# Optimization experiments

Hardware: AMD Instinct MI355X
Metric: run time of the kernel (lower is better)

Reference implementation:

```python
import jax, jax.numpy as jnp
import numpy as np

B, L, D, H = 8, 1500, 1024, 8
HD = D // H
N_BOUNDARIES = 300  # exactly 300 boundaries per sequence -> max_segments = 300
EPS = 1e-5


def setup_inputs() -> dict:
    key = jax.random.key(0)
    ks = jax.random.split(key, 6)
    rng = np.random.default_rng(0)
    boundaries = np.zeros((B, L), dtype=np.float32)
    for b in range(B):
        boundaries[b, rng.permutation(L)[:N_BOUNDARIES]] = 1.0
    lengths = rng.uniform(0.5, 1.0, size=(B,)).astype(np.float32)
    hidden = jax.random.normal(ks[0], (B, L, D), jnp.float32)
    learned_query = jax.random.normal(ks[1], (D,), jnp.float32) * 0.02
    eye = jnp.eye(D, dtype=jnp.float32)
    # identity-initialized projections, perturbed so the test is non-trivial
    Wk = eye + 0.02 * jax.random.normal(ks[2], (D, D), jnp.float32)
    Wv = eye + 0.02 * jax.random.normal(ks[3], (D, D), jnp.float32)
    Wo = eye + 0.02 * jax.random.normal(ks[4], (D, D), jnp.float32)
    return {
        'hidden': hidden,
        'boundaries': jnp.asarray(boundaries),
        'lengths': jnp.asarray(lengths),
        'learned_query': learned_query,
        'Wk': Wk, 'Wv': Wv, 'Wo': Wo,
        'ln_gamma': jnp.ones((D,), jnp.float32),
        'ln_beta': jnp.zeros((D,), jnp.float32),
        'max_segments': N_BOUNDARIES,
    }


def _attention_pooling(hidden, boundaries, lengths, learned_query, Wk, Wv, Wo,
                       ln_gamma, ln_beta, max_segments):
    # segment id per token: cumsum(b) - b (token before first boundary -> seg 0)
    seg_id = jnp.cumsum(boundaries, axis=1) - boundaries            # (B, L)
    # foo[b,t,s] = s - seg_id[b,t]; foo == 0 -> token t belongs to segment s
    seg_mask = (jnp.arange(max_segments)[None, None, :] == seg_id[:, :, None])
    actual_lens = (lengths * L).astype(jnp.int32)                   # (B,)
    len_mask = jnp.arange(L)[None, :] < actual_lens[:, None]        # (B, L)
    seg_mask = seg_mask & len_mask[:, :, None]                      # (B, L, S) bool

    # LayerNorm (biased variance, as torch.nn.LayerNorm)
    mu = jnp.mean(hidden, axis=-1, keepdims=True)
    var = jnp.var(hidden, axis=-1, keepdims=True)
    hn = (hidden - mu) * jax.lax.rsqrt(var + EPS) * ln_gamma + ln_beta

    k = (hn @ Wk.T).reshape(B, L, H, HD)
    v = (hn @ Wv.T).reshape(B, L, H, HD)
    q = learned_query.reshape(H, HD)
    # queries are the same learned vector for every segment -> compute (B,H,L)
    # once and broadcast across S (same math as the original dense matmul)
    scores = jnp.einsum('hd,blhd->bhl', q, k) * (HD ** -0.5)        # (B, H, L)

    mask = seg_mask.transpose(0, 2, 1)[:, None, :, :]               # (B, 1, S, L)
    scores4 = jnp.where(mask, scores[:, :, None, :], -1e30)         # (B, H, S, L)
    w = jax.nn.softmax(scores4, axis=-1)
    w = jnp.where(mask, w, 0.0)
    # rows with no valid token: softmax of all -inf -> nan_to_num(0) in torch
    row_valid = jnp.any(mask, axis=-1, keepdims=True)
    w = jnp.where(row_valid, w, 0.0)

    pooled = jnp.einsum('bhsl,blhd->bshd', w, v).reshape(B, max_segments, D)
    return pooled @ Wo.T                                            # (B, S, D)


def reference(hidden, boundaries, lengths, learned_query, Wk, Wv, Wo,
              ln_gamma, ln_beta, max_segments):
    return _attention_pooling(hidden, boundaries, lengths, learned_query,
                              Wk, Wv, Wo, ln_gamma, ln_beta, max_segments)
```

## Files before the change

kernel.cpp:

```cpp
#include <hip/hip_runtime.h>
#include <hip/hip_bf16.h>

#define BPK_B 8
#define BPK_L 1500
#define BPK_D 1024
#define BPK_H 8
#define BPK_S 300
#define BPK_EPS 1e-5f
#define BPK_M (BPK_B * BPK_L)
#define BPK_MS (BPK_B * BPK_S)
#define BPK_HP_ROWS 2432
#define BPK_PO_PAD 2560

typedef __hip_bfloat16 bf16;
typedef __bf16 bf16x8 __attribute__((ext_vector_type(8)));
typedef float v4f __attribute__((ext_vector_type(4)));

static __device__ __forceinline__ float bf_lo(unsigned u) {
    return __uint_as_float((u & 0xffffu) << 16);
}
static __device__ __forceinline__ float bf_hi(unsigned u) {
    return __uint_as_float((u >> 16) << 16);
}
static __device__ __forceinline__ void bpk_store(float v, float* p) { *p = v; }
static __device__ __forceinline__ void bpk_store(float v, bf16* p) { *p = __float2bfloat16(v); }
static __device__ __forceinline__ uint2 pack4bf(float a, float b, float c, float d) {
    union { bf16 h[4]; uint2 u; } pk;
    pk.h[0] = __float2bfloat16(a); pk.h[1] = __float2bfloat16(b);
    pk.h[2] = __float2bfloat16(c); pk.h[3] = __float2bfloat16(d);
    return pk.u;
}

#define BPK_GL2LDS(gsrc, ldst)                                                 \
    __builtin_amdgcn_global_load_lds(                                          \
        (const __attribute__((address_space(1))) void*)(gsrc),                 \
        (__attribute__((address_space(3))) void*)(ldst), 16, 0, 0)

__global__ __launch_bounds__(256) void bpk_prep_kernel(
    const float* __restrict__ lq, const float* __restrict__ Wk,
    const float* __restrict__ boundaries, const float* __restrict__ lengths,
    bf16* __restrict__ qkb, int* __restrict__ seg_start, int* __restrict__ seg_cnt) {
    __shared__ unsigned char flags[1536];
    __shared__ int st_sh[BPK_S + 2];
    __shared__ int wsumi[4];
    int blk = blockIdx.x;
    int tid = threadIdx.x;
    if (blk < 32) {
        int o = blk * 256 + tid;
        int h = o >> 10, k = o & 1023;
        const float* wr = Wk + (size_t)(h * 128) * BPK_D + k;
        const float* qr = lq + h * 128;
        float s = 0.f;
        #pragma unroll 8
        for (int d = 0; d < 128; d++)
            s += qr[d] * wr[(size_t)d * BPK_D];
        qkb[o] = __float2bfloat16(s);
        return;
    }
    int b = blk - 32;
    int alen = (int)(lengths[b] * (float)BPK_L);
    const float* bd = boundaries + (size_t)b * BPK_L;
    for (int t = tid; t < 1536; t += 256)
        flags[t] = (t < BPK_L && bd[t] >= 0.5f) ? 1 : 0;
    for (int s = tid; s < BPK_S + 2; s += 256) st_sh[s] = BPK_L;
    __syncthreads();
    int base = tid * 6;
    int lsum = 0;
    #pragma unroll
    for (int j = 0; j < 6; j++) lsum += flags[base + j];
    int lane = tid & 63, wid = tid >> 6;
    int scan = lsum;
    #pragma unroll
    for (int off = 1; off < 64; off <<= 1) {
        int u = __shfl_up(scan, off);
        if (lane >= off) scan += u;
    }
    if (lane == 63) wsumi[wid] = scan;
    __syncthreads();
    int wbase = 0;
    for (int w = 0; w < wid; w++) wbase += wsumi[w];
    int run = wbase + scan - lsum;
    #pragma unroll
    for (int j = 0; j < 6; j++) {
        int t = base + j;
        if (t < BPK_L) {
            int sid = run;
            if ((t == 0 || flags[t - 1]) && sid <= BPK_S) st_sh[sid] = t;
            if (flags[t]) run++;
        }
    }
    __syncthreads();
    for (int s = tid; s < BPK_S; s += 256) {
        int st = st_sh[s];
        int e = min(st_sh[s + 1], alen);
        int s0 = min(st, alen);
        seg_start[b * BPK_S + s] = st;
        seg_cnt[b * BPK_S + s] = max(0, e - s0);
    }
}

__global__ __launch_bounds__(256) void bpk_ln_score_conv_kernel(
    const float* __restrict__ x, const float* __restrict__ gamma,
    const float* __restrict__ beta, const bf16* __restrict__ qkb,
    const float* __restrict__ lengths,
    const float* __restrict__ Wv, const float* __restrict__ Wo,
    bf16* __restrict__ wvb, bf16* __restrict__ wob,
    float2* __restrict__ murs, float* __restrict__ scores) {
    int tid = threadIdx.x;
    if (blockIdx.x >= 1024) {
        int cb = blockIdx.x - 1024;
        const float* s = cb < 1024 ? Wv : Wo;
        bf16* d = cb < 1024 ? wvb : wob;
        int i = ((cb & 1023) * 256 + tid) * 4;
        float4 v = *(const float4*)(s + i);
        *(uint2*)(d + i) = pack4bf(v.x, v.y, v.z, v.w);
        return;
    }
    int lane = tid & 63, wid = tid >> 6;
    float4 g[4], bb[4];
    uint2 qk[8][4];
    #pragma unroll
    for (int j = 0; j < 4; j++) {
        g[j]  = *(const float4*)(gamma + j * 256 + lane * 4);
        bb[j] = *(const float4*)(beta + j * 256 + lane * 4);
    }
    #pragma unroll
    for (int h = 0; h < 8; h++)
        #pragma unroll
        for (int j = 0; j < 4; j++)
            qk[h][j] = *(const uint2*)(qkb + h * BPK_D + j * 256 + lane * 4);
    float lv = (lane < BPK_B) ? lengths[lane] : 0.f;
    const bool b0 = (lane & 1) != 0;
    const bool b1 = (lane & 2) != 0;
    const bool b2 = (lane & 4) != 0;
    const int head = 4 * (lane & 1) + (lane & 2) + ((lane >> 2) & 1);

    const int nwaves = 1024 * 4;
    for (int row = blockIdx.x * 4 + wid; row < BPK_M; row += nwaves) {
        int b = row / BPK_L, t = row - b * BPK_L;
        float alenf = __shfl(lv, b);
        if (t >= (int)(alenf * (float)BPK_L)) continue;
        const float* xr = x + (size_t)row * BPK_D;
        float4 f[4];
        float s = 0.f, sq = 0.f;
        #pragma unroll
        for (int j = 0; j < 4; j++) {
            f[j] = *(const float4*)(xr + j * 256 + lane * 4);
            s  += f[j].x + f[j].y + f[j].z + f[j].w;
            sq += f[j].x * f[j].x + f[j].y * f[j].y
                + f[j].z * f[j].z + f[j].w * f[j].w;
        }
        #pragma unroll
        for (int off = 1; off < 64; off <<= 1) {
            s  += __shfl_xor(s, off);
            sq += __shfl_xor(sq, off);
        }
        float mu = s * (1.0f / BPK_D);
        float var = sq * (1.0f / BPK_D) - mu * mu;
        float rs = rsqrtf(var + BPK_EPS);
        float p[8];
        #pragma unroll
        for (int h = 0; h < 8; h++) p[h] = 0.f;
        #pragma unroll
        for (int j = 0; j < 4; j++) {
            float h0 = (f[j].x - mu) * rs * g[j].x + bb[j].x;
            float h1 = (f[j].y - mu) * rs * g[j].y + bb[j].y;
            float h2 = (f[j].z - mu) * rs * g[j].z + bb[j].z;
            float h3 = (f[j].w - mu) * rs * g[j].w + bb[j].w;
            #pragma unroll
            for (int h = 0; h < 8; h++) {
                uint2 qv = qk[h][j];
                p[h] += h0 * bf_lo(qv.x) + h1 * bf_hi(qv.x)
                      + h2 * bf_lo(qv.y) + h3 * bf_hi(qv.y);
            }
        }
        #pragma unroll
        for (int r = 0; r < 4; r++) {
            float send = b0 ? p[r] : p[r + 4];
            float recv = __shfl_xor(send, 1);
            p[r]     += b0 ? 0.f : recv;
            p[r + 4] += b0 ? recv : 0.f;
        }
        float q0 = b0 ? p[4] : p[0];
        float q1 = b0 ? p[5] : p[1];
        float q2 = b0 ? p[6] : p[2];
        float q3 = b0 ? p[7] : p[3];
        {
            float send = b1 ? q0 : q2;
            float recv = __shfl_xor(send, 2);
            q0 += b1 ? 0.f : recv;
            q2 += b1 ? recv : 0.f;
            send = b1 ? q1 : q3;
            recv = __shfl_xor(send, 2);
            q1 += b1 ? 0.f : recv;
            q3 += b1 ? recv : 0.f;
        }
        float a = b1 ? q2 : q0;
        float c = b1 ? q3 : q1;
        float send = b2 ? a : c;
        float recv = __shfl_xor(send, 4);
        float v = (b2 ? c : a) + recv;
        v += __shfl_xor(v, 8);
        v += __shfl_xor(v, 16);
        v += __shfl_xor(v, 32);
        if (lane < 8) {
            scores[((size_t)b * BPK_H + head) * BPK_L + t] =
                v * 0.088388347648318447f;
        } else if (lane == 8) {
            murs[row] = make_float2(mu, rs);
        }
    }
}

__global__ __launch_bounds__(256) void bpk_pool_kernel(
    const float* __restrict__ scores, const float* __restrict__ x,
    const float* __restrict__ gamma, const float* __restrict__ beta,
    const float2* __restrict__ murs,
    const int* __restrict__ seg_start, const int* __restrict__ seg_cnt,
    bf16* __restrict__ hpool) {
    int bs = blockIdx.x;
    int b = bs / BPK_S;
    int tid = threadIdx.x;
    int lane = tid & 63, wid = tid >> 6;
    __shared__ float minv[8][2];
    __shared__ float wls[8][128];
    int cnt = seg_cnt[bs], st = seg_start[bs];
    float4 g4 = *(const float4*)(gamma + tid * 4);
    float4 b4 = *(const float4*)(beta + tid * 4);
    float acc[8][4];
    #pragma unroll
    for (int h = 0; h < 8; h++)
        #pragma unroll
        for (int j = 0; j < 4; j++) acc[h][j] = 0.f;
    if (cnt > 0) {
        if (wid == 0) {
            int h = lane & 7, i0 = lane >> 3;
            const float* sc = scores + ((size_t)(b * 8 + h)) * BPK_L + st;
            float m = -1e30f;
            for (int i = i0; i < cnt; i += 8) m = fmaxf(m, sc[i]);
            #pragma unroll
            for (int off = 8; off < 64; off <<= 1) m = fmaxf(m, __shfl_xor(m, off));
            float l = 0.f;
            for (int i = i0; i < cnt; i += 8) l += __expf(sc[i] - m);
            #pragma unroll
            for (int off = 8; off < 64; off <<= 1) l += __shfl_xor(l, off);
            if (i0 == 0) { minv[h][0] = m; minv[h][1] = 1.0f / l; }
        }
        __syncthreads();
        for (int cb = 0; cb < cnt; cb += 128) {
            int cc = min(128, cnt - cb);
            int hh = tid >> 5, i0 = (tid & 31) * 4;
            #pragma unroll
            for (int j = 0; j < 4; j++) {
                int i = i0 + j;
                if (i < cc)
                    wls[hh][i] = __expf(scores[((size_t)(b * 8 + hh)) * BPK_L + st + cb + i]
                                        - minv[hh][0]) * minv[hh][1];
            }
            __syncthreads();
            const float* xp = x + (size_t)(b * BPK_L + st + cb) * BPK_D + tid * 4;
            const float2* mp = murs + (size_t)(b * BPK_L + st + cb);
            for (int i = 0; i < cc; i++) {
                float4 f = *(const float4*)(xp + (size_t)i * BPK_D);
                float2 mr = mp[i];
                float x0 = (f.x - mr.x) * mr.y * g4.x + b4.x;
                float x1 = (f.y - mr.x) * mr.y * g4.y + b4.y;
                float x2 = (f.z - mr.x) * mr.y * g4.z + b4.z;
                float x3 = (f.w - mr.x) * mr.y * g4.w + b4.w;
                #pragma unroll
                for (int h = 0; h < 8; h++) {
                    float w = wls[h][i];
                    acc[h][0] += w * x0; acc[h][1] += w * x1;
                    acc[h][2] += w * x2; acc[h][3] += w * x3;
                }
            }
            __syncthreads();
        }
    }
    #pragma unroll
    for (int h = 0; h < 8; h++)
        *(uint2*)(hpool + ((size_t)h * BPK_HP_ROWS + bs) * BPK_D + tid * 4) =
            pack4bf(acc[h][0], acc[h][1], acc[h][2], acc[h][3]);
}

__global__ __launch_bounds__(256) void bpk_headgemm_kernel(
    const bf16* __restrict__ hpool, const bf16* __restrict__ wvb,
    bf16* __restrict__ pooled) {
    const int mt = blockIdx.x >> 1, nt = blockIdx.x & 1, h = blockIdx.y;
    const int m0 = mt * 64, n0 = nt * 64;
    const bf16* A = hpool + (size_t)h * BPK_HP_ROWS * BPK_D;
    const bf16* W = wvb + (size_t)(h * 128 + n0) * BPK_D;
    __shared__ bf16 As[64][32];
    __shared__ bf16 Bs[64][32];
    const int tid = threadIdx.x;
    const int lane = tid & 63, wid = tid >> 6;
    const int wm = (wid & 1) * 32, wn = (wid >> 1) * 32;
    const int lm = lane & 15, quad = lane >> 4;
    const int rA = wid * 16 + (lane >> 2);
    const int colc = (lane & 3) * 8;

    v4f acc[2][2];
    #pragma unroll
    for (int i = 0; i < 2; i++)
        #pragma unroll
        for (int j = 0; j < 2; j++) acc[i][j] = (v4f){0.f, 0.f, 0.f, 0.f};

    for (int k0 = 0; k0 < BPK_D; k0 += 32) {
        BPK_GL2LDS(&A[(size_t)(m0 + rA) * BPK_D + k0 + colc], &As[wid * 16][0]);
        BPK_GL2LDS(&W[(size_t)rA * BPK_D + k0 + colc], &Bs[wid * 16][0]);
        __syncthreads();
        bf16x8 af[2], bfr[2];
        #pragma unroll
        for (int i = 0; i < 2; i++)
            af[i] = *(const bf16x8*)&As[wm + i * 16 + lm][quad * 8];
        #pragma unroll
        for (int j = 0; j < 2; j++)
            bfr[j] = *(const bf16x8*)&Bs[wn + j * 16 + lm][quad * 8];
        #pragma unroll
        for (int i = 0; i < 2; i++)
            #pragma unroll
            for (int j = 0; j < 2; j++)
                acc[i][j] = __builtin_amdgcn_mfma_f32_16x16x32_bf16(af[i], bfr[j], acc[i][j], 0, 0, 0);
        __syncthreads();
    }
    #pragma unroll
    for (int i = 0; i < 2; i++) {
        int mbase = m0 + wm + i * 16 + quad * 4;
        #pragma unroll
        for (int j = 0; j < 2; j++) {
            int col = h * 128 + n0 + wn + j * 16 + lm;
            #pragma unroll
            for (int r = 0; r < 4; r++) {
                int m = mbase + r;
                if (m < BPK_MS)
                    pooled[(size_t)m * BPK_D + col] = __float2bfloat16(acc[i][j][r]);
            }
        }
    }
}

__global__ __launch_bounds__(256) void bpk_ogemm_kernel(
    const bf16* __restrict__ A, const bf16* __restrict__ W,
    float* __restrict__ O) {
    const int flat = blockIdx.x;
    const int xcd = flat & 7, slot = flat >> 3;
    const int mt = xcd + 8 * (slot >> 4);
    const int nt = slot & 15;
    const int m0 = mt * 64, n0 = nt * 64;
    __shared__ bf16 As[64][32];
    __shared__ bf16 Bs[64][32];
    const int tid = threadIdx.x;
    const int lane = tid & 63, wid = tid >> 6;
    const int wm = (wid & 1) * 32, wn = (wid >> 1) * 32;
    const int lm = lane & 15, quad = lane >> 4;
    const int rA = wid * 16 + (lane >> 2);
    const int colc = (lane & 3) * 8;

    v4f acc[2][2];
    #pragma unroll
    for (int i = 0; i < 2; i++)
        #pragma unroll
        for (int j = 0; j < 2; j++) acc[i][j] = (v4f){0.f, 0.f, 0.f, 0.f};

    for (int k0 = 0; k0 < BPK_D; k0 += 32) {
        BPK_GL2LDS(&A[(size_t)(m0 + rA) * BPK_D + k0 + colc], &As[wid * 16][0]);
        BPK_GL2LDS(&W[(size_t)(n0 + rA) * BPK_D + k0 + colc], &Bs[wid * 16][0]);
        __syncthreads();
        bf16x8 af[2], bfr[2];
        #pragma unroll
        for (int i = 0; i < 2; i++)
            af[i] = *(const bf16x8*)&As[wm + i * 16 + lm][quad * 8];
        #pragma unroll
        for (int j = 0; j < 2; j++)
            bfr[j] = *(const bf16x8*)&Bs[wn + j * 16 + lm][quad * 8];
        #pragma unroll
        for (int i = 0; i < 2; i++)
            #pragma unroll
            for (int j = 0; j < 2; j++)
                acc[i][j] = __builtin_amdgcn_mfma_f32_16x16x32_bf16(af[i], bfr[j], acc[i][j], 0, 0, 0);
        __syncthreads();
    }
    #pragma unroll
    for (int i = 0; i < 2; i++) {
        int mbase = m0 + wm + i * 16 + quad * 4;
        #pragma unroll
        for (int j = 0; j < 2; j++) {
            int col = n0 + wn + j * 16 + lm;
            #pragma unroll
            for (int r = 0; r < 4; r++) {
                int m = mbase + r;
                if (m < BPK_MS) O[(size_t)m * BPK_D + col] = acc[i][j][r];
            }
        }
    }
}

extern "C" void kernel_launch(void* const* d_in, const int* in_sizes, int n_in,
                              void* d_out, int out_size, void* d_ws, size_t ws_size,
                              hipStream_t stream) {
    const float* hidden     = (const float*)d_in[0];
    const float* boundaries = (const float*)d_in[1];
    const float* lengths    = (const float*)d_in[2];
    const float* lq         = (const float*)d_in[3];
    const float* Wk         = (const float*)d_in[4];
    const float* Wv         = (const float*)d_in[5];
    const float* Wo         = (const float*)d_in[6];
    const float* gamma      = (const float*)d_in[7];
    const float* beta       = (const float*)d_in[8];
    float* out              = (float*)d_out;

    char* ws = (char*)d_ws;
    size_t off = 0;
    auto carve = [&](size_t bytes) -> char* {
        char* p = ws + off;
        off += (bytes + 255) & ~(size_t)255;
        return p;
    };
    bf16* hpool    = (bf16*)carve((size_t)BPK_H * BPK_HP_ROWS * BPK_D * sizeof(bf16));
    bf16* pooled   = (bf16*)carve((size_t)BPK_PO_PAD * BPK_D * sizeof(bf16));
    bf16* wvb      = (bf16*)carve((size_t)BPK_D * BPK_D * sizeof(bf16));
    bf16* wob      = (bf16*)carve((size_t)BPK_D * BPK_D * sizeof(bf16));
    bf16* qkb      = (bf16*)carve((size_t)BPK_H * BPK_D * sizeof(bf16));
    float* scores  = (float*)carve((size_t)BPK_B * BPK_H * BPK_L * sizeof(float));
    float2* murs   = (float2*)carve((size_t)BPK_M * sizeof(float2));
    int* seg_start = (int*)carve((size_t)BPK_B * BPK_S * sizeof(int));
    int* seg_cnt   = (int*)carve((size_t)BPK_B * BPK_S * sizeof(int));

    bpk_prep_kernel<<<dim3(40), dim3(256), 0, stream>>>(
        lq, Wk, boundaries, lengths, qkb, seg_start, seg_cnt);
    bpk_ln_score_conv_kernel<<<dim3(3072), dim3(256), 0, stream>>>(
        hidden, gamma, beta, qkb, lengths, Wv, Wo, wvb, wob, murs, scores);
    bpk_pool_kernel<<<dim3(BPK_MS), dim3(256), 0, stream>>>(
        scores, hidden, gamma, beta, murs, seg_start, seg_cnt, hpool);
    bpk_headgemm_kernel<<<dim3(76, BPK_H), dim3(256), 0, stream>>>(
        hpool, wvb, pooled);
    bpk_ogemm_kernel<<<dim3(640), dim3(256), 0, stream>>>(
        pooled, wob, out);
}
```

Baseline: 173.9 us.

## Fuse LayerNorm/score kernel into per-segment pooling with online softmax

Merges the LayerNorm+score kernel and the segment pooling kernel into one kernel. Each segment block now computes LN statistics and per-head scores for its own tokens, keeps them in shared memory, and applies a chunked online softmax. This removes one launch and the global round trip for scores and mean/rstd. In exchange each block copies qk into LDS and reads hidden rows twice, and the weight-conversion blocks now share the same launch.

Result: slower. 218.1 us (+25.4%).

```diff
diff --git a/kernel.cpp b/kernel.cpp
--- a/kernel.cpp
+++ b/kernel.cpp
@@ -22,8 +22,6 @@
 static __device__ __forceinline__ float bf_hi(unsigned u) {
     return __uint_as_float((u >> 16) << 16);
 }
-static __device__ __forceinline__ void bpk_store(float v, float* p) { *p = v; }
-static __device__ __forceinline__ void bpk_store(float v, bf16* p) { *p = __float2bfloat16(v); }
 static __device__ __forceinline__ uint2 pack4bf(float a, float b, float c, float d) {
     union { bf16 h[4]; uint2 u; } pk;
     pk.h[0] = __float2bfloat16(a); pk.h[1] = __float2bfloat16(b);
@@ -99,16 +97,16 @@
     }
 }
 
-__global__ __launch_bounds__(256) void bpk_ln_score_conv_kernel(
+__global__ __launch_bounds__(256) void bpk_lnpool_kernel(
     const float* __restrict__ x, const float* __restrict__ gamma,
     const float* __restrict__ beta, const bf16* __restrict__ qkb,
-    const float* __restrict__ lengths,
     const float* __restrict__ Wv, const float* __restrict__ Wo,
     bf16* __restrict__ wvb, bf16* __restrict__ wob,
-    float2* __restrict__ murs, float* __restrict__ scores) {
+    const int* __restrict__ seg_start, const int* __restrict__ seg_cnt,
+    bf16* __restrict__ hpool) {
     int tid = threadIdx.x;
-    if (blockIdx.x >= 1024) {
-        int cb = blockIdx.x - 1024;
+    if (blockIdx.x >= BPK_MS) {
+        int cb = blockIdx.x - BPK_MS;
         const float* s = cb < 1024 ? Wv : Wo;
         bf16* d = cb < 1024 ? wvb : wob;
         int i = ((cb & 1023) * 256 + tid) * 4;
@@ -116,171 +114,170 @@
         *(uint2*)(d + i) = pack4bf(v.x, v.y, v.z, v.w);
         return;
     }
-    int lane = tid & 63, wid = tid >> 6;
-    float4 g[4], bb[4];
-    uint2 qk[8][4];
-    #pragma unroll
-    for (int j = 0; j < 4; j++) {
-        g[j]  = *(const float4*)(gamma + j * 256 + lane * 4);
-        bb[j] = *(const float4*)(beta + j * 256 + lane * 4);
-    }
-    #pragma unroll
-    for (int h = 0; h < 8; h++)
-        #pragma unroll
-        for (int j = 0; j < 4; j++)
-            qk[h][j] = *(const uint2*)(qkb + h * BPK_D + j * 256 + lane * 4);
-    float lv = (lane < BPK_B) ? lengths[lane] : 0.f;
-    const bool b0 = (lane & 1) != 0;
-    const bool b1 = (lane & 2) != 0;
-    const bool b2 = (lane & 4) != 0;
-    const int head = 4 * (lane & 1) + (lane & 2) + ((lane >> 2) & 1);
-
-    const int nwaves = 1024 * 4;
-    for (int row = blockIdx.x * 4 + wid; row < BPK_M; row += nwaves) {
-        int b = row / BPK_L, t = row - b * BPK_L;
-        float alenf = __shfl(lv, b);
-        if (t >= (int)(alenf * (float)BPK_L)) continue;
-        const float* xr = x + (size_t)row * BPK_D;
-        float4 f[4];
-        float s = 0.f, sq = 0.f;
-        #pragma unroll
-        for (int j = 0; j < 4; j++) {
-            f[j] = *(const float4*)(xr + j * 256 + lane * 4);
-            s  += f[j].x + f[j].y + f[j].z + f[j].w;
-            sq += f[j].x * f[j].x + f[j].y * f[j].y
-                + f[j].z * f[j].z + f[j].w * f[j].w;
-        }
-        #pragma unroll
-        for (int off = 1; off < 64; off <<= 1) {
-            s  += __shfl_xor(s, off);
-            sq += __shfl_xor(sq, off);
-        }
-        float mu = s * (1.0f / BPK_D);
-        float var = sq * (1.0f / BPK_D) - mu * mu;
-        float rs = rsqrtf(var + BPK_EPS);
-        float p[8];
-        #pragma unroll
-        for (int h = 0; h < 8; h++) p[h] = 0.f;
-        #pragma unroll
-        for (int j = 0; j < 4; j++) {
-            float h0 = (f[j].x - mu) * rs * g[j].x + bb[j].x;
-            float h1 = (f[j].y - mu) * rs * g[j].y + bb[j].y;
-            float h2 = (f[j].z - mu) * rs * g[j].z + bb[j].z;
-            float h3 = (f[j].w - mu) * rs * g[j].w + bb[j].w;
-            #pragma unroll
-            for (int h = 0; h < 8; h++) {
-                uint2 qv = qk[h][j];
-                p[h] += h0 * bf_lo(qv.x) + h1 * bf_hi(qv.x)
-                      + h2 * bf_lo(qv.y) + h3 * bf_hi(qv.y);
-            }
-        }
-        #pragma unroll
-        for (int r = 0; r < 4; r++) {
-            float send = b0 ? p[r] : p[r + 4];
-            float recv = __shfl_xor(send, 1);
-            p[r]     += b0 ? 0.f : recv;
-            p[r + 4] += b0 ? recv : 0.f;
-        }
-        float q0 = b0 ? p[4] : p[0];
-        float q1 = b0 ? p[5] : p[1];
-        float q2 = b0 ? p[6] : p[2];
-        float q3 = b0 ? p[7] : p[3];
-        {
-            float send = b1 ? q0 : q2;
-            float recv = __shfl_xor(send, 2);
-            q0 += b1 ? 0.f : recv;
-            q2 += b1 ? recv : 0.f;
-            send = b1 ? q1 : q3;
-            recv = __shfl_xor(send, 2);
-            q1 += b1 ? 0.f : recv;
-            q3 += b1 ? recv : 0.f;
-        }
-        float a = b1 ? q2 : q0;
-        float c = b1 ? q3 : q1;
-        float send = b2 ? a : c;
-        float recv = __shfl_xor(send, 4);
-        float v = (b2 ? c : a) + recv;
-        v += __shfl_xor(v, 8);
-        v += __shfl_xor(v, 16);
-        v += __shfl_xor(v, 32);
-        if (lane < 8) {
-            scores[((size_t)b * BPK_H + head) * BPK_L + t] =
-                v * 0.088388347648318447f;
-        } else if (lane == 8) {
-            murs[row] = make_float2(mu, rs);
-        }
-    }
-}
-
-__global__ __launch_bounds__(256) void bpk_pool_kernel(
-    const float* __restrict__ scores, const float* __restrict__ x,
-    const float* __restrict__ gamma, const float* __restrict__ beta,
-    const float2* __restrict__ murs,
-    const int* __restrict__ seg_start, const int* __restrict__ seg_cnt,
-    bf16* __restrict__ hpool) {
+    __shared__ bf16 qks[BPK_H * BPK_D];
+    __shared__ float sch[8][128];
+    __shared__ float mch[128][2];
+    __shared__ float wls[8][128];
+    __shared__ float mstate[8], lstate[8], asc[8], csum[8];
     int bs = blockIdx.x;
     int b = bs / BPK_S;
-    int tid = threadIdx.x;
     int lane = tid & 63, wid = tid >> 6;
-    __shared__ float minv[8][2];
-    __shared__ float wls[8][128];
-    int cnt = seg_cnt[bs], st = seg_start[bs];
+    for (int i = tid; i < (BPK_H * BPK_D) / 8; i += 256)
+        ((uint4*)qks)[i] = ((const uint4*)qkb)[i];
+    float4 gw[4], bw[4];
+    #pragma unroll
+    for (int j = 0; j < 4; j++) {
+        gw[j] = *(const float4*)(gamma + j * 256 + lane * 4);
+        bw[j] = *(const float4*)(beta + j * 256 + lane * 4);
+    }
     float4 g4 = *(const float4*)(gamma + tid * 4);
     float4 b4 = *(const float4*)(beta + tid * 4);
+    int cnt = seg_cnt[bs], st = seg_start[bs];
     float acc[8][4];
     #pragma unroll
     for (int h = 0; h < 8; h++)
         #pragma unroll
         for (int j = 0; j < 4; j++) acc[h][j] = 0.f;
-    if (cnt > 0) {
+    if (tid < 8) { mstate[tid] = -3.0e38f; lstate[tid] = 0.f; }
+    const bool bb0 = (lane & 1) != 0;
+    const bool bb1 = (lane & 2) != 0;
+    const bool bb2 = (lane & 4) != 0;
+    const int head = 4 * (lane & 1) + (lane & 2) + ((lane >> 2) & 1);
+    __syncthreads();
+
+    for (int c0 = 0; c0 < cnt; c0 += 128) {
+        int cc = min(128, cnt - c0);
+        for (int i = wid; i < cc; i += 4) {
+            const float* xr = x + (size_t)(b * BPK_L + st + c0 + i) * BPK_D;
+            float4 f[4];
+            float s = 0.f, sq = 0.f;
+            #pragma unroll
+            for (int j = 0; j < 4; j++) {
+                f[j] = *(const float4*)(xr + j * 256 + lane * 4);
+                s  += f[j].x + f[j].y + f[j].z + f[j].w;
+                sq += f[j].x * f[j].x + f[j].y * f[j].y
+                    + f[j].z * f[j].z + f[j].w * f[j].w;
+            }
+            #pragma unroll
+            for (int off = 1; off < 64; off <<= 1) {
+                s  += __shfl_xor(s, off);
+                sq += __shfl_xor(sq, off);
+            }
+            float mu = s * (1.0f / BPK_D);
+            float var = sq * (1.0f / BPK_D) - mu * mu;
+            float rs = rsqrtf(var + BPK_EPS);
+            float p[8];
+            #pragma unroll
+            for (int h = 0; h < 8; h++) p[h] = 0.f;
+            #pragma unroll
+            for (int j = 0; j < 4; j++) {
+                float h0 = (f[j].x - mu) * rs * gw[j].x + bw[j].x;
+                float h1 = (f[j].y - mu) * rs * gw[j].y + bw[j].y;
+                float h2 = (f[j].z - mu) * rs * gw[j].z + bw[j].z;
+                float h3 = (f[j].w - mu) * rs * gw[j].w + bw[j].w;
+                #pragma unroll
+                for (int h = 0; h < 8; h++) {
+                    uint2 qv = *(const uint2*)(qks + h * BPK_D + j * 256 + lane * 4);
+                    p[h] += h0 * bf_lo(qv.x) + h1 * bf_hi(qv.x)
+                          + h2 * bf_lo(qv.y) + h3 * bf_hi(qv.y);
+                }
+            }
+            #pragma unroll
+            for (int r = 0; r < 4; r++) {
+                float send = bb0 ? p[r] : p[r + 4];
+                float recv = __shfl_xor(send, 1);
+                p[r]     += bb0 ? 0.f : recv;
+                p[r + 4] += bb0 ? recv : 0.f;
+            }
+            float q0 = bb0 ? p[4] : p[0];
+            float q1 = bb0 ? p[5] : p[1];
+            float q2 = bb0 ? p[6] : p[2];
+            float q3 = bb0 ? p[7] : p[3];
+            {
+                float send = bb1 ? q0 : q2;
+                float recv = __shfl_xor(send, 2);
+                q0 += bb1 ? 0.f : recv;
+                q2 += bb1 ? recv : 0.f;
+                send = bb1 ? q1 : q3;
+                recv = __shfl_xor(send, 2);
+                q1 += bb1 ? 0.f : recv;
+                q3 += bb1 ? recv : 0.f;
+            }
+            float a = bb1 ? q2 : q0;
+            float c = bb1 ? q3 : q1;
+            float send = bb2 ? a : c;
+            float recv = __shfl_xor(send, 4);
+            float v = (bb2 ? c : a) + recv;
+            v += __shfl_xor(v, 8);
+            v += __shfl_xor(v, 16);
+            v += __shfl_xor(v, 32);
+            if (lane < 8) sch[head][i] = v * 0.088388347648318447f;
+            else if (lane == 8) { mch[i][0] = mu; mch[i][1] = rs; }
+        }
+        __syncthreads();
         if (wid == 0) {
             int h = lane & 7, i0 = lane >> 3;
-            const float* sc = scores + ((size_t)(b * 8 + h)) * BPK_L + st;
-            float m = -1e30f;
-            for (int i = i0; i < cnt; i += 8) m = fmaxf(m, sc[i]);
+            float m = -3.0e38f;
+            for (int i = i0; i < cc; i += 8) m = fmaxf(m, sch[h][i]);
             #pragma unroll
             for (int off = 8; off < 64; off <<= 1) m = fmaxf(m, __shfl_xor(m, off));
-            float l = 0.f;
-            for (int i = i0; i < cnt; i += 8) l += __expf(sc[i] - m);
-            #pragma unroll
-            for (int off = 8; off < 64; off <<= 1) l += __shfl_xor(l, off);
-            if (i0 == 0) { minv[h][0] = m; minv[h][1] = 1.0f / l; }
-        }
-        __syncthreads();
-        for (int cb = 0; cb < cnt; cb += 128) {
-            int cc = min(128, cnt - cb);
+            if (i0 == 0) {
+                float mo = mstate[h];
+                float mn = fmaxf(mo, m);
+                mstate[h] = mn;
+                asc[h] = __expf(mo - mn);
+            }
+        }
+        __syncthreads();
+        {
             int hh = tid >> 5, i0 = (tid & 31) * 4;
+            float mn = mstate[hh];
+            float ps = 0.f;
             #pragma unroll
             for (int j = 0; j < 4; j++) {
                 int i = i0 + j;
-                if (i < cc)
-                    wls[hh][i] = __expf(scores[((size_t)(b * 8 + hh)) * BPK_L + st + cb + i]
-                                        - minv[hh][0]) * minv[hh][1];
-            }
-            __syncthreads();
-            const float* xp = x + (size_t)(b * BPK_L + st + cb) * BPK_D + tid * 4;
-            const float2* mp = murs + (size_t)(b * BPK_L + st + cb);
-            for (int i = 0; i < cc; i++) {
-                float4 f = *(const float4*)(xp + (size_t)i * BPK_D);
-                float2 mr = mp[i];
-                float x0 = (f.x - mr.x) * mr.y * g4.x + b4.x;
-                float x1 = (f.y - mr.x) * mr.y * g4.y + b4.y;
-                float x2 = (f.z - mr.x) * mr.y * g4.z + b4.z;
-                float x3 = (f.w - mr.x) * mr.y * g4.w + b4.w;
-                #pragma unroll
-                for (int h = 0; h < 8; h++) {
-                    float w = wls[h][i];
-                    acc[h][0] += w * x0; acc[h][1] += w * x1;
-                    acc[h][2] += w * x2; acc[h][3] += w * x3;
+                if (i < cc) {
+                    float w = __expf(sch[hh][i] - mn);
+                    wls[hh][i] = w;
+                    ps += w;
                 }
             }
-            __syncthreads();
-        }
-    }
-    #pragma unroll
-    for (int h = 0; h < 8; h++)
+            #pragma unroll
+            for (int off = 1; off < 32; off <<= 1) ps += __shfl_xor(ps, off);
+            if ((tid & 31) == 0) csum[hh] = ps;
+        }
+        __syncthreads();
+        float av[8];
+        #pragma unroll
+        for (int h = 0; h < 8; h++) av[h] = asc[h];
+        #pragma unroll
+        for (int h = 0; h < 8; h++)
+            #pragma unroll
+            for (int j = 0; j < 4; j++) acc[h][j] *= av[h];
+        if (tid < 8) lstate[tid] = lstate[tid] * asc[tid] + csum[tid];
+        const float* xp = x + (size_t)(b * BPK_L + st + c0) * BPK_D + tid * 4;
+        for (int i = 0; i < cc; i++) {
+            float4 f = *(const float4*)(xp + (size_t)i * BPK_D);
+            float mu = mch[i][0], rs = mch[i][1];
+            float x0 = (f.x - mu) * rs * g4.x + b4.x;
+            float x1 = (f.y - mu) * rs * g4.y + b4.y;
+            float x2 = (f.z - mu) * rs * g4.z + b4.z;
+            float x3 = (f.w - mu) * rs * g4.w + b4.w;
+            #pragma unroll
+            for (int h = 0; h < 8; h++) {
+                float w = wls[h][i];
+                acc[h][0] += w * x0; acc[h][1] += w * x1;
+                acc[h][2] += w * x2; acc[h][3] += w * x3;
+            }
+        }
+        __syncthreads();
+    }
+    #pragma unroll
+    for (int h = 0; h < 8; h++) {
+        float inv = (cnt > 0) ? 1.0f / lstate[h] : 0.f;
         *(uint2*)(hpool + ((size_t)h * BPK_HP_ROWS + bs) * BPK_D + tid * 4) =
-            pack4bf(acc[h][0], acc[h][1], acc[h][2], acc[h][3]);
+            pack4bf(acc[h][0] * inv, acc[h][1] * inv, acc[h][2] * inv, acc[h][3] * inv);
+    }
 }
 
 __global__ __launch_bounds__(256) void bpk_headgemm_kernel(
@@ -421,17 +418,13 @@
     bf16* wvb      = (bf16*)carve((size_t)BPK_D * BPK_D * sizeof(bf16));
     bf16* wob      = (bf16*)carve((size_t)BPK_D * BPK_D * sizeof(bf16));
     bf16* qkb      = (bf16*)carve((size_t)BPK_H * BPK_D * sizeof(bf16));
-    float* scores  = (float*)carve((size_t)BPK_B * BPK_H * BPK_L * sizeof(float));
-    float2* murs   = (float2*)carve((size_t)BPK_M * sizeof(float2));
     int* seg_start = (int*)carve((size_t)BPK_B * BPK_S * sizeof(int));
     int* seg_cnt   = (int*)carve((size_t)BPK_B * BPK_S * sizeof(int));
 
     bpk_prep_kernel<<<dim3(40), dim3(256), 0, stream>>>(
         lq, Wk, boundaries, lengths, qkb, seg_start, seg_cnt);
-    bpk_ln_score_conv_kernel<<<dim3(3072), dim3(256), 0, stream>>>(
-        hidden, gamma, beta, qkb, lengths, Wv, Wo, wvb, wob, murs, scores);
-    bpk_pool_kernel<<<dim3(BPK_MS), dim3(256), 0, stream>>>(
-        scores, hidden, gamma, beta, murs, seg_start, seg_cnt, hpool);
+    bpk_lnpool_kernel<<<dim3(BPK_MS + 2048), dim3(256), 0, stream>>>(
+        hidden, gamma, beta, qkb, Wv, Wo, wvb, wob, seg_start, seg_cnt, hpool);
     bpk_headgemm_kernel<<<dim3(76, BPK_H), dim3(256), 0, stream>>>(
         hpool, wvb, pooled);
     bpk_ogemm_kernel<<<dim3(640), dim3(256), 0, stream>>>(
```
